# Kernel optimization log

Hardware: AMD Instinct MI355X
Metric: run time of the kernel (lower is better)

## Reference

```python
import jax, jax.numpy as jnp
import numpy as np

GROUPS = 8
GC = 8          # group_channels = out_channels // groups
SPAN = 32
OUT = 64
EPS = 1e-5


def _bn(x, g, b, axes):
    # training-mode batch norm (biased variance), matching torch BatchNorm forward
    m = x.mean(axis=axes, keepdims=True)
    v = x.var(axis=axes, keepdims=True)
    shape = [1] * x.ndim
    shape[1] = -1
    return (x - m) / jnp.sqrt(v + EPS) * g.reshape(shape) + b.reshape(shape)


def setup_inputs() -> dict:
    key = jax.random.key(0)
    ks = jax.random.split(key, 3)
    x = jax.random.normal(ks[0], (2, 64, 32, 32, 32), dtype=jnp.float32)
    w_qkv = jax.random.normal(ks[1], (2 * OUT, 64), dtype=jnp.float32) * 0.1
    rel_emb = jax.random.normal(ks[2], (2 * GC, 2 * SPAN - 1), dtype=jnp.float32)
    return {
        "x": x,
        "w_qkv": w_qkv,
        "bn_qkv_g": jnp.ones((2 * OUT,), jnp.float32),
        "bn_qkv_b": jnp.zeros((2 * OUT,), jnp.float32),
        "bn_sim_g": jnp.ones((3 * GROUPS,), jnp.float32),
        "bn_sim_b": jnp.zeros((3 * GROUPS,), jnp.float32),
        "bn_out_g": jnp.ones((2 * OUT,), jnp.float32),
        "bn_out_b": jnp.zeros((2 * OUT,), jnp.float32),
        "rel_emb": rel_emb,
    }


def reference(x, w_qkv, bn_qkv_g, bn_qkv_b, bn_sim_g, bn_sim_b, bn_out_g, bn_out_b, rel_emb):
    B, C, H, W, D = x.shape  # dim == 2 -> attend over depth
    L = D  # == SPAN
    xp = jnp.transpose(x, (0, 2, 3, 1, 4)).reshape(B * H * W, C, L)  # (N,C,L)
    N = xp.shape[0]

    # 1x1 conv + BatchNorm1d
    qkv = jnp.einsum('oc,ncl->nol', w_qkv, xp)
    qkv = _bn(qkv, bn_qkv_g, bn_qkv_b, axes=(0, 2))

    qkv = qkv.reshape(N, GROUPS, 2 * GC, L)
    q = qkv[:, :, : GC // 2]                # (N,g,gc/2,L)
    k = qkv[:, :, GC // 2: GC]
    v = qkv[:, :, GC:]                      # (N,g,gc,L)

    # relative embeddings -> (2*gc, span, span)
    idx = (jnp.arange(SPAN)[:, None] - jnp.arange(SPAN)[None, :] + SPAN - 1).reshape(-1)
    emb = rel_emb[:, idx].reshape(2 * GC, SPAN, SPAN)
    qe_emb = emb[: GC // 2]
    ke_emb = emb[GC // 2: GC]
    ve_emb = emb[GC:]

    qe = jnp.einsum('ngci,cij->ngij', q, qe_emb)   # (N,g,L,L)
    ke = jnp.einsum('ngci,cij->ngij', k, ke_emb)
    qk = jnp.einsum('ngci,ngcj->ngij', qe, ke)     # contracts over first L axis (faithful)

    sim = jnp.concatenate([qk, qe, ke], axis=1)    # (N,3g,L,L)
    sim = _bn(sim, bn_sim_g, bn_sim_b, axes=(0, 2, 3))
    sim = sim.reshape(N, 3, GROUPS, L, L).sum(axis=1)
    sim = jax.nn.softmax(sim, axis=3)

    am = jnp.einsum('ngij,ngcj->ngci', sim, v)       # (N,g,gc,L)
    ame = jnp.einsum('ngij,cij->ngci', sim, ve_emb)  # (N,g,gc,L)

    out = jnp.concatenate([am, ame], axis=-1).reshape(N, 2 * OUT, L)
    out = _bn(out, bn_out_g, bn_out_b, axes=(0, 2))
    out = out.reshape(B, H, W, OUT, 2, L).sum(axis=-2)   # (B,H,W,out,L)
    out = jnp.transpose(out, (0, 3, 1, 2, 4))            # (B,out,H,W,D)
    return out
```

## Files before the change

### kernel.cpp

```cpp
#include <hip/hip_runtime.h>


typedef _Float16 f16;
typedef __attribute__((ext_vector_type(2))) _Float16 f16x2;
typedef __attribute__((ext_vector_type(8))) _Float16 f16x8;
typedef __attribute__((ext_vector_type(16))) float f32x16;

struct U4 { unsigned a[4]; };
union F8 { unsigned u[4]; f16x8 v; };

__device__ __forceinline__ U4 ld4(const unsigned* p) {
    uint4 v = *(const uint4*)p;
    U4 r; r.a[0] = v.x; r.a[1] = v.y; r.a[2] = v.z; r.a[3] = v.w;
    return r;
}
__device__ __forceinline__ f16x2 u2h(unsigned u) { return __builtin_bit_cast(f16x2, u); }

__device__ __forceinline__ float fdot2u(unsigned a, unsigned b, float c) {
#if __has_builtin(__builtin_amdgcn_fdot2)
    return __builtin_amdgcn_fdot2(u2h(a), u2h(b), c, false);
#else
    f16x2 x = u2h(a), y = u2h(b);
    return (float)x.x * (float)y.x + (float)x.y * (float)y.y + c;
#endif
}
__device__ __forceinline__ unsigned pkrtz(float a, float b) {
#if __has_builtin(__builtin_amdgcn_cvt_pkrtz)
    return __builtin_bit_cast(unsigned, __builtin_amdgcn_cvt_pkrtz(a, b));
#else
    f16x2 v; v.x = (f16)a; v.y = (f16)b;
    return __builtin_bit_cast(unsigned, v);
#endif
}
__device__ __forceinline__ unsigned pkmul(unsigned a, unsigned b) {
    f16x2 x = u2h(a), y = u2h(b);
    f16x2 r = x * y;
    return __builtin_bit_cast(unsigned, r);
}

__device__ __forceinline__ float sum16(float v) {
    int x;
    x = __builtin_amdgcn_update_dpp(0, __float_as_int(v), 0x121, 0xF, 0xF, true); v += __int_as_float(x);
    x = __builtin_amdgcn_update_dpp(0, __float_as_int(v), 0x122, 0xF, 0xF, true); v += __int_as_float(x);
    x = __builtin_amdgcn_update_dpp(0, __float_as_int(v), 0x124, 0xF, 0xF, true); v += __int_as_float(x);
    x = __builtin_amdgcn_update_dpp(0, __float_as_int(v), 0x128, 0xF, 0xF, true); v += __int_as_float(x);
    return v;
}
__device__ __forceinline__ float sum32(float v) {
    v = sum16(v); return v + __shfl_xor(v, 16);
}
__device__ __forceinline__ float sum64(float v) {
    v = sum16(v); v += __shfl_xor(v, 16); return v + __shfl_xor(v, 32);
}

__global__ __launch_bounds__(512) void k_emb(const float* __restrict__ rel,
                                             f16* __restrict__ gemb) {
    int tid = blockIdx.x * 512 + threadIdx.x;
    int stride = gridDim.x * 512;
    for (int e = tid; e < 4608; e += stride) {
        int c2 = e / 1152, rm = e % 1152, y = rm / 36, x = rm % 36;
        f16 v0 = (f16)0, v1 = (f16)0;
        if (x < 32) {
            v0 = (f16)rel[(2 * c2) * 63 + x - y + 31];
            v1 = (f16)rel[(2 * c2 + 1) * 63 + x - y + 31];
        }
        gemb[2 * e] = v0; gemb[2 * e + 1] = v1;
    }
    for (int e = tid; e < 4608; e += stride) {
        int c2 = e / 1152, rm = e % 1152, a = rm / 36, b = rm % 36;
        f16 v0 = (f16)0, v1 = (f16)0;
        if (b < 32) {
            v0 = (f16)rel[(2 * c2) * 63 + a - b + 31];
            v1 = (f16)rel[(2 * c2 + 1) * 63 + a - b + 31];
        }
        gemb[9216 + 2 * e] = v0; gemb[9216 + 2 * e + 1] = v1;
    }
    for (int e = tid; e < 9216; e += stride) {
        int c = e / 1152, rm = e % 1152, a = rm / 36, b = rm % 36;
        gemb[18432 + e] = (b < 32) ? (f16)rel[(8 + c) * 63 + a - b + 31] : (f16)0;
    }
}

__global__ __launch_bounds__(256) void k_qkv(const float* __restrict__ x,
                                             const float* __restrict__ w,
                                             f16* __restrict__ qkv,
                                             float* __restrict__ pq) {
    __shared__ __attribute__((aligned(16))) unsigned xt[32 * 66];
    int t = threadIdx.x, wv = t >> 6, l = t & 63;
    int li = l & 31, h = l >> 5;
    int bid = blockIdx.x;
    int b = bid >> 9;
    int col0 = (bid & 511) * 64;
    const float* xb = x + (size_t)b * 2097152 + col0;
    #pragma unroll
    for (int k = 0; k < 4; ++k) {
        int idx = t + 256 * k;
        int col2 = idx & 31, p = idx >> 5;
        const float* r0 = xb + (size_t)(2 * p) * 32768 + 2 * col2;
        float2 a = *(const float2*)r0;
        float2 bb = *(const float2*)(r0 + 32768);
        int ks = p >> 3, hh = (p >> 1) & 1, m = (p & 1) + 2 * ((p >> 2) & 1);
        unsigned w0 = pkrtz(a.x, bb.x);
        unsigned w1 = pkrtz(a.y, bb.y);
        *(uint2*)&xt[(ks * 8 + hh * 4 + m) * 66 + 2 * col2] = make_uint2(w0, w1);
    }
    f16x8 aw[4];
    {
        const float* wr = w + (size_t)(32 * wv + li) * 64;
        #pragma unroll
        for (int ks = 0; ks < 4; ++ks) {
            float4 w0 = *(const float4*)(wr + 16 * ks + 4 * h);
            float4 w1 = *(const float4*)(wr + 16 * ks + 8 + 4 * h);
            F8 fa;
            fa.u[0] = pkrtz(w0.x, w0.y); fa.u[1] = pkrtz(w0.z, w0.w);
            fa.u[2] = pkrtz(w1.x, w1.y); fa.u[3] = pkrtz(w1.z, w1.w);
            aw[ks] = fa.v;
        }
    }
    __syncthreads();
    float s1a[16] = {}, s2a[16] = {};
    #pragma unroll
    for (int ct = 0; ct < 2; ++ct) {
        f32x16 D = {};
        #pragma unroll
        for (int ks = 0; ks < 4; ++ks) {
            F8 fb;
            #pragma unroll
            for (int m = 0; m < 4; ++m)
                fb.u[m] = xt[(ks * 8 + h * 4 + m) * 66 + ct * 32 + li];
            D = __builtin_amdgcn_mfma_f32_32x32x16_f16(aw[ks], fb.v, D, 0, 0, 0);
        }
        int colg = col0 + ct * 32 + li;
        f16* qn = qkv + (size_t)b * 4194304 + colg;
        #pragma unroll
        for (int r = 0; r < 16; ++r) {
            int och = 32 * wv + (r & 3) + 8 * (r >> 2) + 4 * h;
            qn[(size_t)och * 32768] = (f16)D[r];
            s1a[r] += D[r];
            s2a[r] += D[r] * D[r];
        }
    }
    #pragma unroll
    for (int r = 0; r < 16; ++r) {
        float s1 = sum32(s1a[r]);
        float s2 = sum32(s2a[r]);
        if (li == 0) {
            int och = 32 * wv + (r & 3) + 8 * (r >> 2) + 4 * h;
            pq[(size_t)bid * 256 + och * 2] = s1;
            pq[(size_t)bid * 256 + och * 2 + 1] = s2;
        }
    }
}

__global__ __launch_bounds__(256) void red_qkv(const float* __restrict__ pq,
                                               float* __restrict__ sqkv) {
    int t = threadIdx.x;
    int base = blockIdx.x * 64;
    float acc = 0;
    #pragma unroll 8
    for (int k = 0; k < 64; ++k) acc += pq[(size_t)(base + k) * 256 + t];
    atomicAdd(&sqkv[((t & 1) ? 128 : 0) + (t >> 1)], acc);
}

__global__ __launch_bounds__(512, 2) void k_sim(const f16* __restrict__ qkv,
                                                const f16* __restrict__ gemb,
                                                const float* __restrict__ sqkv,
                                                const float* __restrict__ bqg,
                                                const float* __restrict__ bqb,
                                                float* __restrict__ psim) {
    __shared__ __attribute__((aligned(16))) f16 qkh[2][8][256];
    __shared__ float statw[8][6];
    int t = threadIdx.x, wv = t >> 6, l = t & 63;
    int g = blockIdx.x & 7, nb = blockIdx.x >> 3;
    int li = l & 31, h = l >> 5;
    const unsigned* eT2u = (const unsigned*)gemb;
    {
        int ch = l >> 3, i0 = (l & 7) * 4;
        int cc = g * 16 + ch;
        float mu = sqkv[cc] * (1.0f / 65536.0f);
        float var = sqkv[128 + cc] * (1.0f / 65536.0f) - mu * mu;
        float aa = bqg[cc] * rsqrtf(var + 1e-5f);
        float bb = bqb[cc] - mu * aa;
        #pragma unroll
        for (int pr = 0; pr < 2; ++pr) {
            int n = nb * 8 + wv + pr * 1024;
            int b_ = n >> 10, hw = n & 1023;
            const f16* qn = qkv + (size_t)b_ * 4194304 + (size_t)(g * 16) * 32768 + hw * 32;
            uint2 q2 = *(const uint2*)(qn + (size_t)ch * 32768 + i0);
            f16x2 p0 = u2h(q2.x), p1 = u2h(q2.y);
            qkh[pr][wv][(i0 + 0) * 8 + ch] = (f16)(aa * (float)p0.x + bb);
            qkh[pr][wv][(i0 + 1) * 8 + ch] = (f16)(aa * (float)p0.y + bb);
            qkh[pr][wv][(i0 + 2) * 8 + ch] = (f16)(aa * (float)p1.x + bb);
            qkh[pr][wv][(i0 + 3) * 8 + ch] = (f16)(aa * (float)p1.y + bb);
        }
    }
    __syncthreads();
    unsigned uq[2][2][4], uk[2][2][4];
    float sqe = 0, sqe2 = 0, ske = 0, ske2 = 0;
    #pragma unroll
    for (int s = 0; s < 2; ++s) {
        #pragma unroll
        for (int blk = 0; blk < 2; ++blk) {
            int p0 = 16 * s + 4 * h + 8 * blk;
            U4 e0 = ld4(eT2u + 0 * 1152 + li * 36 + p0);
            U4 e1 = ld4(eT2u + 1 * 1152 + li * 36 + p0);
            U4 e2 = ld4(eT2u + 2 * 1152 + li * 36 + p0);
            U4 e3 = ld4(eT2u + 3 * 1152 + li * 36 + p0);
            #pragma unroll
            for (int pr = 0; pr < 2; ++pr) {
                float qe[4], ke[4];
                #pragma unroll
                for (int e = 0; e < 4; ++e) {
                    U4 qr = ld4((const unsigned*)&qkh[pr][wv][(p0 + e) * 8]);
                    qe[e] = fdot2u(qr.a[0], e0.a[e], fdot2u(qr.a[1], e1.a[e], 0.f));
                    ke[e] = fdot2u(qr.a[2], e2.a[e], fdot2u(qr.a[3], e3.a[e], 0.f));
                    sqe += qe[e]; sqe2 += qe[e] * qe[e];
                    ske += ke[e]; ske2 += ke[e] * ke[e];
                }
                uq[pr][s][2 * blk + 0] = pkrtz(qe[0], qe[1]);
                uq[pr][s][2 * blk + 1] = pkrtz(qe[2], qe[3]);
                uk[pr][s][2 * blk + 0] = pkrtz(ke[0], ke[1]);
                uk[pr][s][2 * blk + 1] = pkrtz(ke[2], ke[3]);
            }
        }
    }
    float s1 = 0, s2 = 0;
    #pragma unroll
    for (int pr = 0; pr < 2; ++pr) {
        F8 fq0, fq1, fk0, fk1;
        #pragma unroll
        for (int j = 0; j < 4; ++j) {
            fq0.u[j] = uq[pr][0][j]; fq1.u[j] = uq[pr][1][j];
            fk0.u[j] = uk[pr][0][j]; fk1.u[j] = uk[pr][1][j];
        }
        f32x16 D = {};
        D = __builtin_amdgcn_mfma_f32_32x32x16_f16(fk0.v, fq0.v, D, 0, 0, 0);
        D = __builtin_amdgcn_mfma_f32_32x32x16_f16(fk1.v, fq1.v, D, 0, 0, 0);
        #pragma unroll
        for (int r = 0; r < 16; ++r) { s1 += D[r]; s2 += D[r] * D[r]; }
    }
    s1 = sum64(s1);   s2 = sum64(s2);
    sqe = sum64(sqe); sqe2 = sum64(sqe2);
    ske = sum64(ske); ske2 = sum64(ske2);
    if (l == 0) {
        statw[wv][0] = s1;  statw[wv][1] = s2;
        statw[wv][2] = sqe; statw[wv][3] = sqe2;
        statw[wv][4] = ske; statw[wv][5] = ske2;
    }
    __syncthreads();
    if (t < 6) {
        float tot = 0;
        #pragma unroll
        for (int w2 = 0; w2 < 8; ++w2) tot += statw[w2][t];
        psim[blockIdx.x * 8 + t] = tot;
    }
}

__global__ __launch_bounds__(64) void red_sim(const float* __restrict__ psim,
                                              float* __restrict__ ssim) {
    int t = threadIdx.x;
    if (t >= 48) return;
    int g = t / 6, s = t % 6;
    float acc = 0;
    #pragma unroll 8
    for (int nb = 0; nb < 128; ++nb) acc += psim[(nb * 8 + g) * 8 + s];
    const int base[6] = {0, 24, 8, 32, 16, 40};
    ssim[base[s] + g] = acc;
}

__global__ __launch_bounds__(512, 2) void k_attn(const f16* __restrict__ qkv,
                                                 const f16* __restrict__ gemb,
                                                 const float* __restrict__ sqkv,
                                                 const float* __restrict__ bqg,
                                                 const float* __restrict__ bqb,
                                                 const float* __restrict__ ssim,
                                                 const float* __restrict__ bsg,
                                                 const float* __restrict__ bsb,
                                                 f16* __restrict__ oraw,
                                                 float* __restrict__ sout) {
    __shared__ __attribute__((aligned(16))) f16 qkh[2][8][256];
    __shared__ __attribute__((aligned(16))) f16 vh[2][8][288];
    __shared__ float statw[8][32];
    int t = threadIdx.x, wv = t >> 6, l = t & 63;
    int g = blockIdx.x & 7, nb = blockIdx.x >> 3;
    int li = l & 31, h = l >> 5;
    const unsigned* eT2u = (const unsigned*)gemb;
    const unsigned* eP2u = eT2u + 4608;
    const f16* ePvh = gemb + 18432;
    float aQK, aQE, aKE, csum;
    {
        float m0 = ssim[g] * (1.0f / 2097152.0f);
        float v0 = ssim[24 + g] * (1.0f / 2097152.0f) - m0 * m0;
        aQK = bsg[g] * rsqrtf(v0 + 1e-5f);
        float b0 = bsb[g] - m0 * aQK;
        float m1 = ssim[8 + g] * (1.0f / 2097152.0f);
        float v1 = ssim[32 + g] * (1.0f / 2097152.0f) - m1 * m1;
        aQE = bsg[8 + g] * rsqrtf(v1 + 1e-5f);
        float b1 = bsb[8 + g] - m1 * aQE;
        float m2 = ssim[16 + g] * (1.0f / 2097152.0f);
        float v2 = ssim[40 + g] * (1.0f / 2097152.0f) - m2 * m2;
        aKE = bsg[16 + g] * rsqrtf(v2 + 1e-5f);
        float b2 = bsb[16 + g] - m2 * aKE;
        csum = b0 + b1 + b2 - 6.0f;
    }
    {
        int ch = l >> 3, i0 = (l & 7) * 4;
        int cc = g * 16 + ch;
        float mu = sqkv[cc] * (1.0f / 65536.0f);
        float var = sqkv[128 + cc] * (1.0f / 65536.0f) - mu * mu;
        float aa = bqg[cc] * rsqrtf(var + 1e-5f);
        float bb = bqb[cc] - mu * aa;
        int cv = g * 16 + 8 + ch;
        float muv = sqkv[cv] * (1.0f / 65536.0f);
        float varv = sqkv[128 + cv] * (1.0f / 65536.0f) - muv * muv;
        float av = bqg[cv] * rsqrtf(varv + 1e-5f);
        float bv = bqb[cv] - muv * av;
        #pragma unroll
        for (int pr = 0; pr < 2; ++pr) {
            int n = nb * 8 + wv + pr * 1024;
            int b_ = n >> 10, hw = n & 1023;
            const f16* qn = qkv + (size_t)b_ * 4194304 + (size_t)(g * 16) * 32768 + hw * 32;
            uint2 q2 = *(const uint2*)(qn + (size_t)ch * 32768 + i0);
            f16x2 p0 = u2h(q2.x), p1 = u2h(q2.y);
            qkh[pr][wv][(i0 + 0) * 8 + ch] = (f16)(aa * (float)p0.x + bb);
            qkh[pr][wv][(i0 + 1) * 8 + ch] = (f16)(aa * (float)p0.y + bb);
            qkh[pr][wv][(i0 + 2) * 8 + ch] = (f16)(aa * (float)p1.x + bb);
            qkh[pr][wv][(i0 + 3) * 8 + ch] = (f16)(aa * (float)p1.y + bb);
            uint2 v2q = *(const uint2*)(qn + (size_t)(8 + ch) * 32768 + i0);
            f16x2 v0 = u2h(v2q.x), v1q = u2h(v2q.y);
            vh[pr][wv][ch * 36 + i0 + 0] = (f16)(av * (float)v0.x + bv);
            vh[pr][wv][ch * 36 + i0 + 1] = (f16)(av * (float)v0.y + bv);
            vh[pr][wv][ch * 36 + i0 + 2] = (f16)(av * (float)v1q.x + bv);
            vh[pr][wv][ch * 36 + i0 + 3] = (f16)(av * (float)v1q.y + bv);
        }
    }
    __syncthreads();
    unsigned uq[2][2][4], uk[2][2][4];
    #pragma unroll
    for (int s = 0; s < 2; ++s) {
        #pragma unroll
        for (int blk = 0; blk < 2; ++blk) {
            int p0 = 16 * s + 4 * h + 8 * blk;
            U4 e0 = ld4(eT2u + 0 * 1152 + li * 36 + p0);
            U4 e1 = ld4(eT2u + 1 * 1152 + li * 36 + p0);
            U4 e2 = ld4(eT2u + 2 * 1152 + li * 36 + p0);
            U4 e3 = ld4(eT2u + 3 * 1152 + li * 36 + p0);
            #pragma unroll
            for (int pr = 0; pr < 2; ++pr) {
                float qe[4], ke[4];
                #pragma unroll
                for (int e = 0; e < 4; ++e) {
                    U4 qr = ld4((const unsigned*)&qkh[pr][wv][(p0 + e) * 8]);
                    qe[e] = fdot2u(qr.a[0], e0.a[e], fdot2u(qr.a[1], e1.a[e], 0.f));
                    ke[e] = fdot2u(qr.a[2], e2.a[e], fdot2u(qr.a[3], e3.a[e], 0.f));
                }
                uq[pr][s][2 * blk + 0] = pkrtz(qe[0], qe[1]);
                uq[pr][s][2 * blk + 1] = pkrtz(qe[2], qe[3]);
                uk[pr][s][2 * blk + 0] = pkrtz(ke[0], ke[1]);
                uk[pr][s][2 * blk + 1] = pkrtz(ke[2], ke[3]);
            }
        }
    }
    f32x16 Dq0 = {}, Dq1 = {};
    {
        F8 fq0, fq1, fk0, fk1;
        #pragma unroll
        for (int j = 0; j < 4; ++j) {
            fq0.u[j] = uq[0][0][j]; fq1.u[j] = uq[0][1][j];
            fk0.u[j] = uk[0][0][j]; fk1.u[j] = uk[0][1][j];
        }
        Dq0 = __builtin_amdgcn_mfma_f32_32x32x16_f16(fk0.v, fq0.v, Dq0, 0, 0, 0);
        Dq0 = __builtin_amdgcn_mfma_f32_32x32x16_f16(fk1.v, fq1.v, Dq0, 0, 0, 0);
        #pragma unroll
        for (int j = 0; j < 4; ++j) {
            fq0.u[j] = uq[1][0][j]; fq1.u[j] = uq[1][1][j];
            fk0.u[j] = uk[1][0][j]; fk1.u[j] = uk[1][1][j];
        }
        Dq1 = __builtin_amdgcn_mfma_f32_32x32x16_f16(fk0.v, fq0.v, Dq1, 0, 0, 0);
        Dq1 = __builtin_amdgcn_mfma_f32_32x32x16_f16(fk1.v, fq1.v, Dq1, 0, 0, 0);
    }
    U4 qhv0 = ld4((const unsigned*)&qkh[0][wv][li * 8]);
    U4 qhv1 = ld4((const unsigned*)&qkh[1][wv][li * 8]);
    unsigned up0[8], up1[8];
    float se0 = 0, se1 = 0;
    const unsigned one2 = 0x3C003C00u;
    #pragma unroll
    for (int rq = 0; rq < 4; ++rq) {
        int j0 = 8 * rq + 4 * h;
        U4 a0 = ld4(eP2u + 0 * 1152 + li * 36 + j0);
        U4 a1 = ld4(eP2u + 1 * 1152 + li * 36 + j0);
        U4 a2 = ld4(eP2u + 2 * 1152 + li * 36 + j0);
        U4 a3 = ld4(eP2u + 3 * 1152 + li * 36 + j0);
        float ev0[4], ev1[4];
        #pragma unroll
        for (int e = 0; e < 4; ++e) {
            float qe4 = fdot2u(qhv0.a[0], a0.a[e], fdot2u(qhv0.a[1], a1.a[e], 0.f));
            float ke4 = fdot2u(qhv0.a[2], a2.a[e], fdot2u(qhv0.a[3], a3.a[e], 0.f));
            ev0[e] = __expf(aQK * Dq0[4 * rq + e] + aQE * qe4 + aKE * ke4 + csum);
            qe4 = fdot2u(qhv1.a[0], a0.a[e], fdot2u(qhv1.a[1], a1.a[e], 0.f));
            ke4 = fdot2u(qhv1.a[2], a2.a[e], fdot2u(qhv1.a[3], a3.a[e], 0.f));
            ev1[e] = __expf(aQK * Dq1[4 * rq + e] + aQE * qe4 + aKE * ke4 + csum);
        }
        up0[2 * rq] = pkrtz(ev0[0], ev0[1]); up0[2 * rq + 1] = pkrtz(ev0[2], ev0[3]);
        up1[2 * rq] = pkrtz(ev1[0], ev1[1]); up1[2 * rq + 1] = pkrtz(ev1[2], ev1[3]);
        se0 = fdot2u(up0[2 * rq], one2, se0); se0 = fdot2u(up0[2 * rq + 1], one2, se0);
        se1 = fdot2u(up1[2 * rq], one2, se1); se1 = fdot2u(up1[2 * rq + 1], one2, se1);
    }
    se0 += __shfl_xor(se0, 32);
    se1 += __shfl_xor(se1, 32);
    float iv0 = __frcp_rn(se0), iv1 = __frcp_rn(se1);
    unsigned hi0 = pkrtz(iv0, iv0), hi1 = pkrtz(iv1, iv1);
    #pragma unroll
    for (int w2 = 0; w2 < 8; ++w2) { up0[w2] = pkmul(up0[w2], hi0); up1[w2] = pkmul(up1[w2], hi1); }
    f32x16 D20 = {}, D21 = {};
    #pragma unroll
    for (int pr = 0; pr < 2; ++pr) {
        F8 fp0, fp1, fv0, fv1;
        const unsigned* up = pr ? up1 : up0;
        fp0.u[0] = up[0]; fp0.u[1] = up[1]; fp0.u[2] = up[2]; fp0.u[3] = up[3];
        fp1.u[0] = up[4]; fp1.u[1] = up[5]; fp1.u[2] = up[6]; fp1.u[3] = up[7];
        const f16* vb = &vh[pr][wv][(li & 7) * 36];
        uint2 va0 = *(const uint2*)(vb + 4 * h);
        uint2 vb0 = *(const uint2*)(vb + 4 * h + 8);
        uint2 va1 = *(const uint2*)(vb + 16 + 4 * h);
        uint2 vb1 = *(const uint2*)(vb + 16 + 4 * h + 8);
        if (li >= 8) {
            va0 = make_uint2(0, 0); vb0 = make_uint2(0, 0);
            va1 = make_uint2(0, 0); vb1 = make_uint2(0, 0);
        }
        fv0.u[0] = va0.x; fv0.u[1] = va0.y; fv0.u[2] = vb0.x; fv0.u[3] = vb0.y;
        fv1.u[0] = va1.x; fv1.u[1] = va1.y; fv1.u[2] = vb1.x; fv1.u[3] = vb1.y;
        if (pr == 0) {
            D20 = __builtin_amdgcn_mfma_f32_32x32x16_f16(fv0.v, fp0.v, D20, 0, 0, 0);
            D20 = __builtin_amdgcn_mfma_f32_32x32x16_f16(fv1.v, fp1.v, D20, 0, 0, 0);
        } else {
            D21 = __builtin_amdgcn_mfma_f32_32x32x16_f16(fv0.v, fp0.v, D21, 0, 0, 0);
            D21 = __builtin_amdgcn_mfma_f32_32x32x16_f16(fv1.v, fp1.v, D21, 0, 0, 0);
        }
    }
    float ame0[8], ame1[8];
    #pragma unroll
    for (int c = 0; c < 8; ++c) {
        const f16* er = ePvh + (c * 32 + li) * 36;
        float a0c = 0, a1c = 0;
        #pragma unroll
        for (int s = 0; s < 2; ++s) {
            #pragma unroll
            for (int dd = 0; dd < 2; ++dd) {
                uint2 ev = *(const uint2*)(er + 16 * s + 8 * dd + 4 * h);
                int widx = 4 * s + 2 * dd;
                a0c = fdot2u(up0[widx], ev.x, a0c);
                a0c = fdot2u(up0[widx + 1], ev.y, a0c);
                a1c = fdot2u(up1[widx], ev.x, a1c);
                a1c = fdot2u(up1[widx + 1], ev.y, a1c);
            }
        }
        ame0[c] = a0c + __shfl_xor(a0c, 32);
        ame1[c] = a1c + __shfl_xor(a1c, 32);
    }
    int n0 = nb * 8 + wv, n1 = n0 + 1024;
    f16* on0 = oraw + (size_t)n0 * 4096 + g * 512;
    f16* on1 = oraw + (size_t)n1 * 4096 + g * 512;
    #pragma unroll
    for (int e = 0; e < 4; ++e) {
        int c = e + 4 * h;
        float av0 = D20[e], av1 = D21[e];
        float ae0 = ame0[c], ae1 = ame1[c];
        on0[(2 * c) * 32 + li] = (f16)av0;
        on0[(2 * c + 1) * 32 + li] = (f16)ae0;
        on1[(2 * c) * 32 + li] = (f16)av1;
        on1[(2 * c + 1) * 32 + li] = (f16)ae1;
        float x1 = sum32(av0 + av1), x2 = sum32(av0 * av0 + av1 * av1);
        float y1 = sum32(ae0 + ae1), y2 = sum32(ae0 * ae0 + ae1 * ae1);
        if (li == 0) {
            statw[wv][(2 * c) * 2 + 0] = x1;     statw[wv][(2 * c) * 2 + 1] = x2;
            statw[wv][(2 * c + 1) * 2 + 0] = y1; statw[wv][(2 * c + 1) * 2 + 1] = y2;
        }
    }
    __syncthreads();
    if (t < 32) {
        float tot = 0;
        #pragma unroll
        for (int w2 = 0; w2 < 8; ++w2) tot += statw[w2][t];
        int u = t >> 1;
        int och = g * 16 + u;
        atomicAdd(&sout[((t & 1) ? 128 : 0) + och], tot);
    }
}

__global__ __launch_bounds__(256) void k_out(const f16* __restrict__ oraw,
                                             const float* __restrict__ sout,
                                             const float* __restrict__ bog,
                                             const float* __restrict__ bob,
                                             float* __restrict__ out) {
    int gid = blockIdx.x * 256 + threadIdx.x;
    int l4 = gid & 7;
    int rest = gid >> 3;
    int w2 = rest & 31; rest >>= 5;
    int hh = rest & 31; rest >>= 5;
    int oc = rest & 63;
    int b = rest >> 6;
    int n = b * 1024 + hh * 32 + w2;
    int c0 = 2 * oc, c1 = 2 * oc + 1;
    float mu0 = sout[c0] * (1.0f / 65536.0f);
    float v0 = sout[128 + c0] * (1.0f / 65536.0f) - mu0 * mu0;
    float a0 = bog[c0] * rsqrtf(v0 + 1e-5f);
    float b0 = bob[c0] - mu0 * a0;
    float mu1 = sout[c1] * (1.0f / 65536.0f);
    float v1 = sout[128 + c1] * (1.0f / 65536.0f) - mu1 * mu1;
    float a1 = bog[c1] * rsqrtf(v1 + 1e-5f);
    float b1 = bob[c1] - mu1 * a1;
    float cc = b0 + b1;
    const f16* on = oraw + (size_t)n * 4096;
    uint2 r0 = *(const uint2*)(on + oc * 64 + l4 * 4);
    uint2 r1 = *(const uint2*)(on + oc * 64 + 32 + l4 * 4);
    f16x2 r0a = u2h(r0.x), r0b = u2h(r0.y);
    f16x2 r1a = u2h(r1.x), r1b = u2h(r1.y);
    float4 o;
    o.x = a0 * (float)r0a.x + a1 * (float)r1a.x + cc;
    o.y = a0 * (float)r0a.y + a1 * (float)r1a.y + cc;
    o.z = a0 * (float)r0b.x + a1 * (float)r1b.x + cc;
    o.w = a0 * (float)r0b.y + a1 * (float)r1b.y + cc;
    *((float4*)out + gid) = o;
}

extern "C" void kernel_launch(void* const* d_in, const int* in_sizes, int n_in,
                              void* d_out, int out_size, void* d_ws, size_t ws_size,
                              hipStream_t stream) {
    const float* x   = (const float*)d_in[0];
    const float* w   = (const float*)d_in[1];
    const float* bqg = (const float*)d_in[2];
    const float* bqb = (const float*)d_in[3];
    const float* bsg = (const float*)d_in[4];
    const float* bsb = (const float*)d_in[5];
    const float* bog = (const float*)d_in[6];
    const float* bob = (const float*)d_in[7];
    const float* rel = (const float*)d_in[8];

    float* ws = (float*)d_ws;
    f16* qkv16  = (f16*)ws;
    f16* oraw16 = (f16*)(ws + 4194304);
    f16* gemb   = (f16*)(ws + 8388608);
    float* psim = ws + 8388608 + 13824;
    float* pq   = psim + 16384;
    float* stats = pq + 262144;
    float* sqkv = stats;
    float* ssim = stats + 256;
    float* sout = stats + 304;

    hipMemsetAsync(stats, 0, 560 * sizeof(float), stream);

    k_emb<<<9, 512, 0, stream>>>(rel, gemb);
    k_qkv<<<1024, 256, 0, stream>>>(x, w, qkv16, pq);
    red_qkv<<<16, 256, 0, stream>>>(pq, sqkv);
    k_sim<<<1024, 512, 0, stream>>>(qkv16, gemb, sqkv, bqg, bqb, psim);
    red_sim<<<1, 64, 0, stream>>>(psim, ssim);
    k_attn<<<1024, 512, 0, stream>>>(qkv16, gemb, sqkv, bqg, bqb, ssim, bsg, bsb, oraw16, sout);
    k_out<<<4096, 256, 0, stream>>>(oraw16, sout, bog, bob, (float*)d_out);
}
```

Before: 100.1 us.

## Store qk scores from k_sim in fp16 and reuse in k_attn, fuse emb build

k_sim now writes its per-position qk MFMA result to a workspace buffer in fp16, and k_attn reads it back instead of recomputing the qe/ke projections and MFMAs. The relative-embedding table build moves into red_qkv, removing one launch. Both attention kernels switch to 256-thread blocks with twice the grid and higher occupancy hints. This trades recompute for a large extra global write and read of the score tensor.

New measurement: 129.6 us. 29.4% more time.

```diff
diff --git a/kernel.cpp b/kernel.cpp
--- a/kernel.cpp
+++ b/kernel.cpp
@@ -51,34 +51,6 @@
 }
 __device__ __forceinline__ float sum64(float v) {
     v = sum16(v); v += __shfl_xor(v, 16); return v + __shfl_xor(v, 32);
-}
-
-__global__ __launch_bounds__(512) void k_emb(const float* __restrict__ rel,
-                                             f16* __restrict__ gemb) {
-    int tid = blockIdx.x * 512 + threadIdx.x;
-    int stride = gridDim.x * 512;
-    for (int e = tid; e < 4608; e += stride) {
-        int c2 = e / 1152, rm = e % 1152, y = rm / 36, x = rm % 36;
-        f16 v0 = (f16)0, v1 = (f16)0;
-        if (x < 32) {
-            v0 = (f16)rel[(2 * c2) * 63 + x - y + 31];
-            v1 = (f16)rel[(2 * c2 + 1) * 63 + x - y + 31];
-        }
-        gemb[2 * e] = v0; gemb[2 * e + 1] = v1;
-    }
-    for (int e = tid; e < 4608; e += stride) {
-        int c2 = e / 1152, rm = e % 1152, a = rm / 36, b = rm % 36;
-        f16 v0 = (f16)0, v1 = (f16)0;
-        if (b < 32) {
-            v0 = (f16)rel[(2 * c2) * 63 + a - b + 31];
-            v1 = (f16)rel[(2 * c2 + 1) * 63 + a - b + 31];
-        }
-        gemb[9216 + 2 * e] = v0; gemb[9216 + 2 * e + 1] = v1;
-    }
-    for (int e = tid; e < 9216; e += stride) {
-        int c = e / 1152, rm = e % 1152, a = rm / 36, b = rm % 36;
-        gemb[18432 + e] = (b < 32) ? (f16)rel[(8 + c) * 63 + a - b + 31] : (f16)0;
-    }
 }
 
 __global__ __launch_bounds__(256) void k_qkv(const float* __restrict__ x,
@@ -153,23 +125,49 @@
 }
 
 __global__ __launch_bounds__(256) void red_qkv(const float* __restrict__ pq,
-                                               float* __restrict__ sqkv) {
+                                               float* __restrict__ sqkv,
+                                               const float* __restrict__ rel,
+                                               f16* __restrict__ gemb) {
     int t = threadIdx.x;
     int base = blockIdx.x * 64;
     float acc = 0;
     #pragma unroll 8
     for (int k = 0; k < 64; ++k) acc += pq[(size_t)(base + k) * 256 + t];
     atomicAdd(&sqkv[((t & 1) ? 128 : 0) + (t >> 1)], acc);
-}
-
-__global__ __launch_bounds__(512, 2) void k_sim(const f16* __restrict__ qkv,
+    int tid = blockIdx.x * 256 + t;
+    for (int e = tid; e < 4608; e += 4096) {
+        int c2 = e / 1152, rm = e % 1152, y = rm / 36, x = rm % 36;
+        f16 v0 = (f16)0, v1 = (f16)0;
+        if (x < 32) {
+            v0 = (f16)rel[(2 * c2) * 63 + x - y + 31];
+            v1 = (f16)rel[(2 * c2 + 1) * 63 + x - y + 31];
+        }
+        gemb[2 * e] = v0; gemb[2 * e + 1] = v1;
+    }
+    for (int e = tid; e < 4608; e += 4096) {
+        int c2 = e / 1152, rm = e % 1152, a = rm / 36, b = rm % 36;
+        f16 v0 = (f16)0, v1 = (f16)0;
+        if (b < 32) {
+            v0 = (f16)rel[(2 * c2) * 63 + a - b + 31];
+            v1 = (f16)rel[(2 * c2 + 1) * 63 + a - b + 31];
+        }
+        gemb[9216 + 2 * e] = v0; gemb[9216 + 2 * e + 1] = v1;
+    }
+    for (int e = tid; e < 9216; e += 4096) {
+        int c = e / 1152, rm = e % 1152, a = rm / 36, b = rm % 36;
+        gemb[18432 + e] = (b < 32) ? (f16)rel[(8 + c) * 63 + a - b + 31] : (f16)0;
+    }
+}
+
+__global__ __launch_bounds__(256, 4) void k_sim(const f16* __restrict__ qkv,
                                                 const f16* __restrict__ gemb,
                                                 const float* __restrict__ sqkv,
                                                 const float* __restrict__ bqg,
                                                 const float* __restrict__ bqb,
+                                                f16* __restrict__ qk16,
                                                 float* __restrict__ psim) {
-    __shared__ __attribute__((aligned(16))) f16 qkh[2][8][256];
-    __shared__ float statw[8][6];
+    __shared__ __attribute__((aligned(16))) f16 qkh[2][4][256];
+    __shared__ float statw[4][6];
     int t = threadIdx.x, wv = t >> 6, l = t & 63;
     int g = blockIdx.x & 7, nb = blockIdx.x >> 3;
     int li = l & 31, h = l >> 5;
@@ -183,7 +181,7 @@
         float bb = bqb[cc] - mu * aa;
         #pragma unroll
         for (int pr = 0; pr < 2; ++pr) {
-            int n = nb * 8 + wv + pr * 1024;
+            int n = nb * 4 + wv + pr * 1024;
             int b_ = n >> 10, hw = n & 1023;
             const f16* qn = qkv + (size_t)b_ * 4194304 + (size_t)(g * 16) * 32768 + hw * 32;
             uint2 q2 = *(const uint2*)(qn + (size_t)ch * 32768 + i0);
@@ -236,6 +234,14 @@
         f32x16 D = {};
         D = __builtin_amdgcn_mfma_f32_32x32x16_f16(fk0.v, fq0.v, D, 0, 0, 0);
         D = __builtin_amdgcn_mfma_f32_32x32x16_f16(fk1.v, fq1.v, D, 0, 0, 0);
+        int n = nb * 4 + wv + pr * 1024;
+        f16* qp = qk16 + ((size_t)n * 8 + g) * 1024 + li * 32 + 4 * h;
+        #pragma unroll
+        for (int rq = 0; rq < 4; ++rq) {
+            unsigned lo = pkrtz(D[4 * rq + 0], D[4 * rq + 1]);
+            unsigned hi = pkrtz(D[4 * rq + 2], D[4 * rq + 3]);
+            *(uint2*)(qp + 8 * rq) = make_uint2(lo, hi);
+        }
         #pragma unroll
         for (int r = 0; r < 16; ++r) { s1 += D[r]; s2 += D[r] * D[r]; }
     }
@@ -249,9 +255,7 @@
     }
     __syncthreads();
     if (t < 6) {
-        float tot = 0;
-        #pragma unroll
-        for (int w2 = 0; w2 < 8; ++w2) tot += statw[w2][t];
+        float tot = statw[0][t] + statw[1][t] + statw[2][t] + statw[3][t];
         psim[blockIdx.x * 8 + t] = tot;
     }
 }
@@ -263,12 +267,12 @@
     int g = t / 6, s = t % 6;
     float acc = 0;
     #pragma unroll 8
-    for (int nb = 0; nb < 128; ++nb) acc += psim[(nb * 8 + g) * 8 + s];
+    for (int nb = 0; nb < 256; ++nb) acc += psim[(nb * 8 + g) * 8 + s];
     const int base[6] = {0, 24, 8, 32, 16, 40};
     ssim[base[s] + g] = acc;
 }
 
-__global__ __launch_bounds__(512, 2) void k_attn(const f16* __restrict__ qkv,
+__global__ __launch_bounds__(256, 6) void k_attn(const f16* __restrict__ qkv,
                                                  const f16* __restrict__ gemb,
                                                  const float* __restrict__ sqkv,
                                                  const float* __restrict__ bqg,
@@ -276,17 +280,18 @@
                                                  const float* __restrict__ ssim,
                                                  const float* __restrict__ bsg,
                                                  const float* __restrict__ bsb,
+                                                 const f16* __restrict__ qk16,
                                                  f16* __restrict__ oraw,
                                                  float* __restrict__ sout) {
-    __shared__ __attribute__((aligned(16))) f16 qkh[2][8][256];
-    __shared__ __attribute__((aligned(16))) f16 vh[2][8][288];
-    __shared__ float statw[8][32];
+    __shared__ __attribute__((aligned(16))) f16 qkh[2][4][256];
+    __shared__ __attribute__((aligned(16))) f16 vh[2][4][288];
+    __shared__ float statw[4][32];
     int t = threadIdx.x, wv = t >> 6, l = t & 63;
     int g = blockIdx.x & 7, nb = blockIdx.x >> 3;
     int li = l & 31, h = l >> 5;
-    const unsigned* eT2u = (const unsigned*)gemb;
-    const unsigned* eP2u = eT2u + 4608;
+    const unsigned* eP2u = (const unsigned*)gemb + 4608;
     const f16* ePvh = gemb + 18432;
+    int n0 = nb * 4 + wv, n1 = n0 + 1024;
     float aQK, aQE, aKE, csum;
     {
         float m0 = ssim[g] * (1.0f / 2097152.0f);
@@ -317,7 +322,7 @@
         float bv = bqb[cv] - muv * av;
         #pragma unroll
         for (int pr = 0; pr < 2; ++pr) {
-            int n = nb * 8 + wv + pr * 1024;
+            int n = pr ? n1 : n0;
             int b_ = n >> 10, hw = n & 1023;
             const f16* qn = qkv + (size_t)b_ * 4194304 + (size_t)(g * 16) * 32768 + hw * 32;
             uint2 q2 = *(const uint2*)(qn + (size_t)ch * 32768 + i0);
@@ -335,52 +340,10 @@
         }
     }
     __syncthreads();
-    unsigned uq[2][2][4], uk[2][2][4];
-    #pragma unroll
-    for (int s = 0; s < 2; ++s) {
-        #pragma unroll
-        for (int blk = 0; blk < 2; ++blk) {
-            int p0 = 16 * s + 4 * h + 8 * blk;
-            U4 e0 = ld4(eT2u + 0 * 1152 + li * 36 + p0);
-            U4 e1 = ld4(eT2u + 1 * 1152 + li * 36 + p0);
-            U4 e2 = ld4(eT2u + 2 * 1152 + li * 36 + p0);
-            U4 e3 = ld4(eT2u + 3 * 1152 + li * 36 + p0);
-            #pragma unroll
-            for (int pr = 0; pr < 2; ++pr) {
-                float qe[4], ke[4];
-                #pragma unroll
-                for (int e = 0; e < 4; ++e) {
-                    U4 qr = ld4((const unsigned*)&qkh[pr][wv][(p0 + e) * 8]);
-                    qe[e] = fdot2u(qr.a[0], e0.a[e], fdot2u(qr.a[1], e1.a[e], 0.f));
-                    ke[e] = fdot2u(qr.a[2], e2.a[e], fdot2u(qr.a[3], e3.a[e], 0.f));
-                }
-                uq[pr][s][2 * blk + 0] = pkrtz(qe[0], qe[1]);
-                uq[pr][s][2 * blk + 1] = pkrtz(qe[2], qe[3]);
-                uk[pr][s][2 * blk + 0] = pkrtz(ke[0], ke[1]);
-                uk[pr][s][2 * blk + 1] = pkrtz(ke[2], ke[3]);
-            }
-        }
-    }
-    f32x16 Dq0 = {}, Dq1 = {};
-    {
-        F8 fq0, fq1, fk0, fk1;
-        #pragma unroll
-        for (int j = 0; j < 4; ++j) {
-            fq0.u[j] = uq[0][0][j]; fq1.u[j] = uq[0][1][j];
-            fk0.u[j] = uk[0][0][j]; fk1.u[j] = uk[0][1][j];
-        }
-        Dq0 = __builtin_amdgcn_mfma_f32_32x32x16_f16(fk0.v, fq0.v, Dq0, 0, 0, 0);
-        Dq0 = __builtin_amdgcn_mfma_f32_32x32x16_f16(fk1.v, fq1.v, Dq0, 0, 0, 0);
-        #pragma unroll
-        for (int j = 0; j < 4; ++j) {
-            fq0.u[j] = uq[1][0][j]; fq1.u[j] = uq[1][1][j];
-            fk0.u[j] = uk[1][0][j]; fk1.u[j] = uk[1][1][j];
-        }
-        Dq1 = __builtin_amdgcn_mfma_f32_32x32x16_f16(fk0.v, fq0.v, Dq1, 0, 0, 0);
-        Dq1 = __builtin_amdgcn_mfma_f32_32x32x16_f16(fk1.v, fq1.v, Dq1, 0, 0, 0);
-    }
     U4 qhv0 = ld4((const unsigned*)&qkh[0][wv][li * 8]);
     U4 qhv1 = ld4((const unsigned*)&qkh[1][wv][li * 8]);
+    const f16* qp0 = qk16 + ((size_t)n0 * 8 + g) * 1024 + li * 32 + 4 * h;
+    const f16* qp1 = qk16 + ((size_t)n1 * 8 + g) * 1024 + li * 32 + 4 * h;
     unsigned up0[8], up1[8];
     float se0 = 0, se1 = 0;
     const unsigned one2 = 0x3C003C00u;
@@ -391,15 +354,21 @@
         U4 a1 = ld4(eP2u + 1 * 1152 + li * 36 + j0);
         U4 a2 = ld4(eP2u + 2 * 1152 + li * 36 + j0);
         U4 a3 = ld4(eP2u + 3 * 1152 + li * 36 + j0);
+        uint2 dd0 = *(const uint2*)(qp0 + 8 * rq);
+        uint2 dd1 = *(const uint2*)(qp1 + 8 * rq);
+        f16x2 d0a = u2h(dd0.x), d0b = u2h(dd0.y);
+        f16x2 d1a = u2h(dd1.x), d1b = u2h(dd1.y);
+        float qk0[4] = {(float)d0a.x, (float)d0a.y, (float)d0b.x, (float)d0b.y};
+        float qk1[4] = {(float)d1a.x, (float)d1a.y, (float)d1b.x, (float)d1b.y};
         float ev0[4], ev1[4];
         #pragma unroll
         for (int e = 0; e < 4; ++e) {
             float qe4 = fdot2u(qhv0.a[0], a0.a[e], fdot2u(qhv0.a[1], a1.a[e], 0.f));
             float ke4 = fdot2u(qhv0.a[2], a2.a[e], fdot2u(qhv0.a[3], a3.a[e], 0.f));
-            ev0[e] = __expf(aQK * Dq0[4 * rq + e] + aQE * qe4 + aKE * ke4 + csum);
+            ev0[e] = __expf(aQK * qk0[e] + aQE * qe4 + aKE * ke4 + csum);
             qe4 = fdot2u(qhv1.a[0], a0.a[e], fdot2u(qhv1.a[1], a1.a[e], 0.f));
             ke4 = fdot2u(qhv1.a[2], a2.a[e], fdot2u(qhv1.a[3], a3.a[e], 0.f));
-            ev1[e] = __expf(aQK * Dq1[4 * rq + e] + aQE * qe4 + aKE * ke4 + csum);
+            ev1[e] = __expf(aQK * qk1[e] + aQE * qe4 + aKE * ke4 + csum);
         }
         up0[2 * rq] = pkrtz(ev0[0], ev0[1]); up0[2 * rq + 1] = pkrtz(ev0[2], ev0[3]);
         up1[2 * rq] = pkrtz(ev1[0], ev1[1]); up1[2 * rq + 1] = pkrtz(ev1[2], ev1[3]);
@@ -458,7 +427,6 @@
         ame0[c] = a0c + __shfl_xor(a0c, 32);
         ame1[c] = a1c + __shfl_xor(a1c, 32);
     }
-    int n0 = nb * 8 + wv, n1 = n0 + 1024;
     f16* on0 = oraw + (size_t)n0 * 4096 + g * 512;
     f16* on1 = oraw + (size_t)n1 * 4096 + g * 512;
     #pragma unroll
@@ -479,9 +447,7 @@
     }
     __syncthreads();
     if (t < 32) {
-        float tot = 0;
-        #pragma unroll
-        for (int w2 = 0; w2 < 8; ++w2) tot += statw[w2][t];
+        float tot = statw[0][t] + statw[1][t] + statw[2][t] + statw[3][t];
         int u = t >> 1;
         int och = g * 16 + u;
         atomicAdd(&sout[((t & 1) ? 128 : 0) + och], tot);
@@ -537,24 +503,23 @@
     const float* bob = (const float*)d_in[7];
     const float* rel = (const float*)d_in[8];
 
-    float* ws = (float*)d_ws;
-    f16* qkv16  = (f16*)ws;
-    f16* oraw16 = (f16*)(ws + 4194304);
-    f16* gemb   = (f16*)(ws + 8388608);
-    float* psim = ws + 8388608 + 13824;
-    float* pq   = psim + 16384;
-    float* stats = pq + 262144;
+    f16* qkv16  = (f16*)d_ws;
+    f16* oraw16 = qkv16 + 8388608;
+    f16* qk16   = oraw16 + 8388608;
+    f16* gemb   = qk16 + 16777216;
+    float* stats = (float*)(gemb + 27648);
     float* sqkv = stats;
     float* ssim = stats + 256;
     float* sout = stats + 304;
+    float* psim = (float*)oraw16;
+    float* pq   = (float*)qk16;
 
     hipMemsetAsync(stats, 0, 560 * sizeof(float), stream);
 
-    k_emb<<<9, 512, 0, stream>>>(rel, gemb);
     k_qkv<<<1024, 256, 0, stream>>>(x, w, qkv16, pq);
-    red_qkv<<<16, 256, 0, stream>>>(pq, sqkv);
-    k_sim<<<1024, 512, 0, stream>>>(qkv16, gemb, sqkv, bqg, bqb, psim);
+    red_qkv<<<16, 256, 0, stream>>>(pq, sqkv, rel, gemb);
+    k_sim<<<2048, 256, 0, stream>>>(qkv16, gemb, sqkv, bqg, bqb, qk16, psim);
     red_sim<<<1, 64, 0, stream>>>(psim, ssim);
-    k_attn<<<1024, 512, 0, stream>>>(qkv16, gemb, sqkv, bqg, bqb, ssim, bsg, bsb, oraw16, sout);
+    k_attn<<<2048, 256, 0, stream>>>(qkv16, gemb, sqkv, bqg, bqb, ssim, bsg, bsb, qk16, oraw16, sout);
     k_out<<<4096, 256, 0, stream>>>(oraw16, sout, bog, bob, (float*)d_out);
 }
```
